# Optimization experiments

Hardware: AMD Instinct MI355X
Metric: run time of the kernel (lower is better)

## Reference

```python
import jax, jax.numpy as jnp
import numpy as np

D_MODEL = 1024
N_HEADS = 16
SEQ_LEN = 2048
BATCH = 2
NEG = -1.0e9


def sinusoidal_embeddings(seq_len, d_k):
    # Faithful to the torch version: row 0 is all zeros; even cols get sin,
    # odd cols get cos of position/theta (theta uses the SAME index j, not j//2).
    theta = 10000.0 ** (2.0 * jnp.arange(d_k, dtype=jnp.float32) / d_k)  # [d_k]
    pos = jnp.arange(1, seq_len, dtype=jnp.float32)[:, None] / theta      # [S-1, d_k]
    even = (jnp.arange(d_k) % 2 == 0)
    body = jnp.where(even, jnp.sin(pos), jnp.cos(pos))                    # [S-1, d_k]
    return jnp.concatenate([jnp.zeros((1, d_k), dtype=pos.dtype), body], axis=0)


def setup_inputs() -> dict:
    key = jax.random.key(0)
    k_x, k_q, k_k, k_v, k_o = jax.random.split(key, 5)
    scale = 0.02
    return {
        "X": jax.random.normal(k_x, (BATCH, SEQ_LEN, D_MODEL), dtype=jnp.float32),
        "W_q": jax.random.normal(k_q, (D_MODEL, D_MODEL), dtype=jnp.float32) * scale,
        "W_k": jax.random.normal(k_k, (D_MODEL, D_MODEL), dtype=jnp.float32) * scale,
        "W_v": jax.random.normal(k_v, (D_MODEL, D_MODEL), dtype=jnp.float32) * scale,
        "W_o": jax.random.normal(k_o, (D_MODEL, D_MODEL), dtype=jnp.float32) * scale,
    }


def reference(X, W_q, W_k, W_v, W_o):
    B, S, D = X.shape
    H, d_k = N_HEADS, D // N_HEADS

    def proj(W):  # nn.Linear (no bias): y = x @ W.T, then split heads -> [B,H,S,d_k]
        return (X @ W.T).reshape(B, S, H, d_k).transpose(0, 2, 1, 3)

    Q, K, V = proj(W_q), proj(W_k), proj(W_v)

    pos = sinusoidal_embeddings(S, d_k)          # [S, d_k]
    Q = Q + pos
    K = K + pos

    mask = jnp.triu(jnp.full((S, S), NEG, dtype=X.dtype), k=1)  # [S,S]
    scores = jnp.einsum("bhqd,bhkd->bhqk", Q, K) / jnp.sqrt(jnp.float32(d_k)) + mask
    weights = jax.nn.softmax(scores, axis=-1)
    attn = jnp.einsum("bhqk,bhkd->bhqd", weights, V)            # [B,H,S,d_k]

    attn = attn.transpose(0, 2, 1, 3).reshape(B, S, D)
    return attn @ W_o.T + X
```

## Files before the change

### kernel.cpp

```cpp
#include <hip/hip_runtime.h>
#include <hip/hip_bf16.h>
#include <math.h>

#define S_LEN 2048
#define DMODEL 1024
#define NHEADS 16
#define DHEAD 64
#define NBATCH 2
#define MROWS (NBATCH * S_LEN)

typedef float f32x4 __attribute__((ext_vector_type(4)));
typedef unsigned short u16x8 __attribute__((ext_vector_type(8)));
typedef __bf16 bf16x8 __attribute__((ext_vector_type(8)));

__device__ __forceinline__ f32x4 mfma16(u16x8 a, u16x8 b, f32x4 c) {
    return __builtin_amdgcn_mfma_f32_16x16x32_bf16(
        __builtin_bit_cast(bf16x8, a), __builtin_bit_cast(bf16x8, b), c, 0, 0, 0);
}

__device__ __forceinline__ unsigned short f2bf(float f) {
    unsigned int u = __builtin_bit_cast(unsigned int, f);
    u += 0x7FFFu + ((u >> 16) & 1u);
    return (unsigned short)(u >> 16);
}

__device__ __forceinline__ unsigned int cvtpk(float lo, float hi) {
    unsigned int r;
    asm("v_cvt_pk_bf16_f32 %0, %1, %2" : "=v"(r) : "v"(lo), "v"(hi));
    return r;
}

__device__ __forceinline__ void gl16(const void* g, void* l) {
    __builtin_amdgcn_global_load_lds(
        (const __attribute__((address_space(1))) unsigned int*)g,
        (__attribute__((address_space(3))) unsigned int*)l, 16, 0, 0);
}

#define PIPE_BAR_12() do { \
    asm volatile("s_waitcnt vmcnt(12)" ::: "memory"); \
    __builtin_amdgcn_sched_barrier(0); \
    __builtin_amdgcn_s_barrier(); \
    __builtin_amdgcn_sched_barrier(0); } while (0)
#define PIPE_BAR_0() do { \
    asm volatile("s_waitcnt vmcnt(0)" ::: "memory"); \
    __builtin_amdgcn_sched_barrier(0); \
    __builtin_amdgcn_s_barrier(); \
    __builtin_amdgcn_sched_barrier(0); } while (0)

__global__ __launch_bounds__(256) void cvt5(
    const float* __restrict__ X, const float* __restrict__ Wq,
    const float* __restrict__ Wk, const float* __restrict__ Wv,
    const float* __restrict__ Wo,
    unsigned short* __restrict__ Xbf, unsigned short* __restrict__ Wbf,
    float* __restrict__ pos)
{
    int b = blockIdx.x;
    if (b >= 4096) {
        int i = (b - 4096) * 256 + threadIdx.x;
        int s = i >> 6, d = i & 63;
        float theta = powf(10000.0f, (2.0f * (float)d) / 64.0f);
        float x = (float)s / theta;
        float v = (d & 1) ? cosf(x) : sinf(x);
        pos[i] = (s == 0) ? 0.0f : v;
        return;
    }
    const float* s; unsigned short* d; int t;
    if (b < 2048) { s = X; d = Xbf; t = b * 256 + threadIdx.x; }
    else {
        int z = (b - 2048) >> 9, bb = (b - 2048) & 511;
        s = (z == 0) ? Wq : (z == 1) ? Wk : (z == 2) ? Wv : Wo;
        d = Wbf + (z << 20);
        t = bb * 256 + threadIdx.x;
    }
    float4 a = *((const float4*)s + t * 2);
    float4 c = *((const float4*)s + t * 2 + 1);
    u16x8 o;
    o[0] = f2bf(a.x); o[1] = f2bf(a.y); o[2] = f2bf(a.z); o[3] = f2bf(a.w);
    o[4] = f2bf(c.x); o[5] = f2bf(c.y); o[6] = f2bf(c.z); o[7] = f2bf(c.w);
    *((u16x8*)d + t) = o;
}

__global__ __launch_bounds__(512) void gemm_qkv(
    const unsigned short* __restrict__ Xbf, const unsigned short* __restrict__ Wbf,
    const float* __restrict__ pos,
    unsigned short* __restrict__ qb, unsigned short* __restrict__ kb,
    unsigned short* __restrict__ vt)
{
    const int y = blockIdx.y;
    const int z = y >> 2;
    const unsigned short* __restrict__ W = Wbf + (z << 20);
    __shared__ unsigned short L[2][32768];
    const int t = threadIdx.x;
    const int lane = t & 63;
    const int w = t >> 6;
    const int wm = w >> 2, wn = w & 3;
    const int m0 = blockIdx.x * 256;
    const int nb = (y & 3) * 256;
    const int ll = lane & 15, lg = lane >> 4;
    const int tr = t >> 3;
    const int ch = (t & 7) ^ (tr & 7);

    f32x4 acc[8][4] = {};

    const unsigned short* gA[4];
    const unsigned short* gB[4];
    #pragma unroll
    for (int i = 0; i < 4; i++) {
        gA[i] = Xbf + (m0 + i * 64 + tr) * 1024 + ch * 8;
        gB[i] = W + (nb + i * 64 + tr) * 1024 + ch * 8;
    }

    const int sw0 = ((0 * 4 + lg) ^ (ll & 7)) * 16;
    const int sw1 = ((1 * 4 + lg) ^ (ll & 7)) * 16;
    const int aBase = (wm * 128 + ll) * 128;
    const int bBase = 32768 + (wn * 64 + ll) * 128;

    auto sqA01 = [&](unsigned short* Ln) {
        gl16(gA[0], Ln + (0 * 64 + w * 8) * 64); gA[0] += 64;
        gl16(gA[1], Ln + (1 * 64 + w * 8) * 64); gA[1] += 64;
    };
    auto sqA23 = [&](unsigned short* Ln) {
        gl16(gA[2], Ln + (2 * 64 + w * 8) * 64); gA[2] += 64;
        gl16(gA[3], Ln + (3 * 64 + w * 8) * 64); gA[3] += 64;
    };
    auto sqB01 = [&](unsigned short* Ln) {
        gl16(gB[0], Ln + 16384 + (0 * 64 + w * 8) * 64); gB[0] += 64;
        gl16(gB[1], Ln + 16384 + (1 * 64 + w * 8) * 64); gB[1] += 64;
    };
    auto sqB23 = [&](unsigned short* Ln) {
        gl16(gB[2], Ln + 16384 + (2 * 64 + w * 8) * 64); gB[2] += 64;
        gl16(gB[3], Ln + 16384 + (3 * 64 + w * 8) * 64); gB[3] += 64;
    };

    u16x8 bf[4][2];

    auto quad = [&](int q, const char* bA) {
        const char* pa = bA + aBase + q * 4096;
        u16x8 a00 = *(const u16x8*)(pa + sw0);
        u16x8 a01 = *(const u16x8*)(pa + sw1);
        u16x8 a10 = *(const u16x8*)(pa + 2048 + sw0);
        u16x8 a11 = *(const u16x8*)(pa + 2048 + sw1);
        __builtin_amdgcn_s_setprio(1);
        #pragma unroll
        for (int nf = 0; nf < 4; nf++) {
            acc[q * 2 + 0][nf] = mfma16(a00, bf[nf][0], acc[q * 2 + 0][nf]);
            acc[q * 2 + 1][nf] = mfma16(a10, bf[nf][0], acc[q * 2 + 1][nf]);
        }
        #pragma unroll
        for (int nf = 0; nf < 4; nf++) {
            acc[q * 2 + 0][nf] = mfma16(a01, bf[nf][1], acc[q * 2 + 0][nf]);
            acc[q * 2 + 1][nf] = mfma16(a11, bf[nf][1], acc[q * 2 + 1][nf]);
        }
        __builtin_amdgcn_s_setprio(0);
    };

    auto ktile = [&](const unsigned short* Lb, unsigned short* Ln, bool stg) {
        const char* bA = (const char*)Lb;
        const char* bB = (const char*)Lb;
        if (stg) sqA01(Ln);
        #pragma unroll
        for (int nf = 0; nf < 4; nf++) {
            const char* p = bB + bBase + nf * 2048;
            bf[nf][0] = *(const u16x8*)(p + sw0);
            bf[nf][1] = *(const u16x8*)(p + sw1);
        }
        quad(0, bA);
        __builtin_amdgcn_s_barrier();
        if (stg) sqA23(Ln);
        quad(1, bA);
        __builtin_amdgcn_s_barrier();
        if (stg) sqB01(Ln);
        quad(2, bA);
        __builtin_amdgcn_s_barrier();
        if (stg) sqB23(Ln);
        quad(3, bA);
        PIPE_BAR_0();
    };

    sqA01(L[0]); sqA23(L[0]); sqB01(L[0]); sqB23(L[0]);
    PIPE_BAR_0();
    #pragma unroll 1
    for (int tt = 0; tt < 8; tt++) {
        ktile(L[0], L[1], true);
        ktile(L[1], L[0], tt != 7);
    }

    if (z == 2) {
        #pragma unroll
        for (int mf = 0; mf < 8; mf++) {
            const int row0 = m0 + wm * 128 + mf * 16 + lg * 4;
            const int b = row0 >> 11, s0 = row0 & 2047;
            #pragma unroll
            for (int nf = 0; nf < 4; nf++) {
                const int c = nb + wn * 64 + nf * 16 + ll;
                const int h = c >> 6, d = c & 63;
                unsigned long long pk =
                    (unsigned long long)cvtpk(acc[mf][nf][0], acc[mf][nf][1]) |
                    ((unsigned long long)cvtpk(acc[mf][nf][2], acc[mf][nf][3]) << 32);
                *(unsigned long long*)&vt[(((b * NHEADS + h) * 64) + d) * S_LEN + s0] = pk;
            }
        }
    } else {
        unsigned short* const dst = (z == 0) ? qb : kb;
        #pragma unroll
        for (int mf = 0; mf < 8; mf++) {
            #pragma unroll
            for (int nf = 0; nf < 4; nf++) {
                #pragma unroll
                for (int r = 0; r < 4; r++) {
                    const int row = m0 + wm * 128 + mf * 16 + lg * 4 + r;
                    const int c = nb + wn * 64 + nf * 16 + ll;
                    const int b = row >> 11, s = row & 2047;
                    const int h = c >> 6, d = c & 63;
                    float v = acc[mf][nf][r] + pos[s * 64 + d];
                    if (z == 0) v *= 0.1803368801111244f;
                    dst[(((b * NHEADS + h) * S_LEN) + s) * 64 + d] = f2bf(v);
                }
            }
        }
    }
}

__global__ __launch_bounds__(512, 4) void attn_kernel(
    const unsigned short* __restrict__ qb,
    const unsigned short* __restrict__ kb,
    const unsigned short* __restrict__ vt,
    unsigned short* __restrict__ attnb)
{
    __shared__ unsigned short Klds[2][128 * 64];
    __shared__ unsigned short Vlds[2][64 * 128];
    __shared__ unsigned short Plds[8][16 * 64];

    const int bh = blockIdx.y;
    const int x = blockIdx.x;
    const int qt = (bh < 16) ? (15 - x) : x;

    const int lane = threadIdx.x & 63;
    const int w = threadIdx.x >> 6;
    const int lg = lane >> 4, ll = lane & 15;
    const int r8 = lane >> 3, ch = (lane & 7) ^ r8;
    const int r4 = lane >> 4, c16 = lane & 15;

    const unsigned short* Q = qb + bh * (S_LEN * 64);
    const unsigned short* K = kb + bh * (S_LEN * 64);
    const unsigned short* V = vt + bh * (64 * S_LEN);
    const int q0 = qt * 128 + w * 16;

    u16x8 qf0 = *(const u16x8*)(Q + (q0 + ll) * 64 + lg * 8);
    u16x8 qf1 = *(const u16x8*)(Q + (q0 + ll) * 64 + 32 + lg * 8);

    f32x4 o_acc[4] = {};
    float l_part = 0.0f;

    const int sw0 = ((0 * 4 + lg) ^ (ll & 7)) * 16;
    const int sw1 = ((1 * 4 + lg) ^ (ll & 7)) * 16;
    const char* kb0p0 = (const char*)&Klds[0][0] + ll * 128 + sw0;
    const char* kb0p1 = (const char*)&Klds[0][0] + ll * 128 + sw1;
    const char* kb1p0 = (const char*)&Klds[1][0] + ll * 128 + sw0;
    const char* kb1p1 = (const char*)&Klds[1][0] + ll * 128 + sw1;
    const char* vb0p0 = (const char*)&Vlds[0][0] + ll * 256 + sw0;
    const char* vb0p1 = (const char*)&Vlds[0][0] + ll * 256 + sw1;
    const char* vb1p0 = (const char*)&Vlds[1][0] + ll * 256 + sw0;
    const char* vb1p1 = (const char*)&Vlds[1][0] + ll * 256 + sw1;
    const int E = (ll & 7) << 4;
    char* pwb = (char*)&Plds[w][0] + (((ll * 128) + lg * 8) ^ (E & 16));
    const int pw_o0 = 0 ^ (E & 96), pw_o1 = 32 ^ (E & 96);
    const int pw_o2 = 64 ^ (E & 96), pw_o3 = 96 ^ (E & 96);
    const char* pr0 = (const char*)&Plds[w][0] + ll * 128 + sw0;
    const char* pr1 = (const char*)&Plds[w][0] + ll * 128 + sw1;
    unsigned short* kd0 = &Klds[0][(w * 16) * 64];
    unsigned short* kd1 = &Klds[1][(w * 16) * 64];
    unsigned short* vd0 = &Vlds[0][(w * 8) * 128];
    unsigned short* vd1 = &Vlds[1][(w * 8) * 128];
    const unsigned short* gk  = K + (w * 16 + r8) * 64 + ch * 8;
    const unsigned short* gva = V + (w * 8 + r4) * S_LEN + ((c16 ^ r4) * 8);
    const unsigned short* gvb = V + (w * 8 + 4 + r4) * S_LEN + ((c16 ^ (4 + r4)) * 8);
    const int dthr = w * 16 + ll - lg * 4;

    auto stage2 = [&](unsigned short* kd, unsigned short* vd) {
        gl16(gk, kd);
        gl16(gk + 512, kd + 512);
        gl16(gva, vd);
        gl16(gvb, vd + 512);
        gk += 128 * 64;
        gva += 128;
        gvb += 128;
    };

    auto tile_body = [&](const char* kp0, const char* kp1,
                         const char* vp0, const char* vp1, bool masked, int thr) {
        f32x4 sc[4] = {};
        __builtin_amdgcn_s_setprio(1);
        #pragma unroll
        for (int f = 0; f < 4; f++) {
            const u16x8 kfa = *(const u16x8*)(kp0 + f * 2048);
            sc[f] = mfma16(kfa, qf0, sc[f]);
            const u16x8 kfb = *(const u16x8*)(kp1 + f * 2048);
            sc[f] = mfma16(kfb, qf1, sc[f]);
        }
        __builtin_amdgcn_s_setprio(0);
        if (masked) {
            #pragma unroll
            for (int f = 0; f < 4; f++)
                #pragma unroll
                for (int r = 0; r < 4; r++)
                    if (f * 16 + r > thr) sc[f][r] = -1.0e9f;
        }
        float ts = 0.0f;
        #pragma unroll
        for (int f = 0; f < 4; f++)
            #pragma unroll
            for (int r = 0; r < 4; r++) {
                const float p = __builtin_amdgcn_exp2f(sc[f][r]);
                sc[f][r] = p;
                ts += p;
            }
        l_part += ts;
        *(unsigned long long*)(pwb + pw_o0) =
            (unsigned long long)cvtpk(sc[0][0], sc[0][1]) | ((unsigned long long)cvtpk(sc[0][2], sc[0][3]) << 32);
        *(unsigned long long*)(pwb + pw_o1) =
            (unsigned long long)cvtpk(sc[1][0], sc[1][1]) | ((unsigned long long)cvtpk(sc[1][2], sc[1][3]) << 32);
        *(unsigned long long*)(pwb + pw_o2) =
            (unsigned long long)cvtpk(sc[2][0], sc[2][1]) | ((unsigned long long)cvtpk(sc[2][2], sc[2][3]) << 32);
        *(unsigned long long*)(pwb + pw_o3) =
            (unsigned long long)cvtpk(sc[3][0], sc[3][1]) | ((unsigned long long)cvtpk(sc[3][2], sc[3][3]) << 32);
        const u16x8 pf0 = *(const u16x8*)pr0;
        const u16x8 pf1 = *(const u16x8*)pr1;
        __builtin_amdgcn_s_setprio(1);
        #pragma unroll
        for (int f = 0; f < 4; f++) {
            o_acc[f] = mfma16(pf0, *(const u16x8*)(vp0 + f * 4096), o_acc[f]);
            o_acc[f] = mfma16(pf1, *(const u16x8*)(vp1 + f * 4096), o_acc[f]);
        }
        __builtin_amdgcn_s_setprio(0);
    };

    auto body128_full = [&](const char* kp0, const char* kp1,
                            const char* vp0, const char* vp1) {
        tile_body(kp0, kp1, vp0, vp1, false, 0);
        tile_body(kp0 + 8192, kp1 + 8192, vp0 + 128, vp1 + 128, false, 0);
    };
    auto body128_diag = [&](const char* kp0, const char* kp1,
                            const char* vp0, const char* vp1) {
        tile_body(kp0, kp1, vp0, vp1, true, dthr);
        if (w >= 4)
            tile_body(kp0 + 8192, kp1 + 8192, vp0 + 128, vp1 + 128, true, dthr - 64);
    };

    stage2(kd0, vd0);
    __syncthreads();

    int p = 0;
    while (p + 2 <= qt) {
        stage2(kd1, vd1);
        body128_full(kb0p0, kb0p1, vb0p0, vb0p1);
        __syncthreads();
        stage2(kd0, vd0);
        body128_full(kb1p0, kb1p1, vb1p0, vb1p1);
        __syncthreads();
        p += 2;
    }
    if (p < qt) {
        stage2(kd1, vd1);
        body128_full(kb0p0, kb0p1, vb0p0, vb0p1);
        __syncthreads();
        body128_diag(kb1p0, kb1p1, vb1p0, vb1p1);
    } else {
        body128_diag(kb0p0, kb0p1, vb0p0, vb0p1);
    }

    l_part += __shfl_xor(l_part, 16);
    l_part += __shfl_xor(l_part, 32);

    const int bb = bh >> 4, h = bh & 15;
    float lr0 = 1.0f / __shfl(l_part, lg * 4 + 0);
    float lr1 = 1.0f / __shfl(l_part, lg * 4 + 1);
    float lr2 = 1.0f / __shfl(l_part, lg * 4 + 2);
    float lr3 = 1.0f / __shfl(l_part, lg * 4 + 3);
    #pragma unroll
    for (int f = 0; f < 4; f++) {
        const int colbase = h * 64 + f * 16 + ll;
        attnb[(bb * S_LEN + q0 + lg * 4 + 0) * DMODEL + colbase] = f2bf(o_acc[f][0] * lr0);
        attnb[(bb * S_LEN + q0 + lg * 4 + 1) * DMODEL + colbase] = f2bf(o_acc[f][1] * lr1);
        attnb[(bb * S_LEN + q0 + lg * 4 + 2) * DMODEL + colbase] = f2bf(o_acc[f][2] * lr2);
        attnb[(bb * S_LEN + q0 + lg * 4 + 3) * DMODEL + colbase] = f2bf(o_acc[f][3] * lr3);
    }
}

__global__ __launch_bounds__(128) void gemm_out(
    const unsigned short* __restrict__ Abf,
    const unsigned short* __restrict__ Wbf,
    const float* __restrict__ X,
    float* __restrict__ out)
{
    const unsigned short* __restrict__ W = Wbf + (3u << 20);
    __shared__ unsigned short L[3][192 * 64];
    const int t = threadIdx.x;
    const int lane = t & 63;
    const int w = t >> 6;
    const int m0 = blockIdx.x * 128;
    const int n0 = blockIdx.y * 64;
    const int ll = lane & 15, lg = lane >> 4;
    const int r8 = lane >> 3, ch = (lane & 7) ^ r8;

    f32x4 acc[4][4] = {};

    const unsigned short* gA[8];
    const unsigned short* gB[4];
    #pragma unroll
    for (int i = 0; i < 8; i++) gA[i] = Abf + (m0 + w * 64 + i * 8 + r8) * 1024 + ch * 8;
    #pragma unroll
    for (int i = 0; i < 4; i++) gB[i] = W + (n0 + w * 32 + i * 8 + r8) * 1024 + ch * 8;

    const int sw0 = ((0 * 4 + lg) ^ (ll & 7)) * 16;
    const int sw1 = ((1 * 4 + lg) ^ (ll & 7)) * 16;

    auto stage = [&](unsigned short* Lb) {
        unsigned short* const dA = Lb + (w * 64) * 64;
        unsigned short* const dB = Lb + 128 * 64 + (w * 32) * 64;
        #pragma unroll
        for (int i = 0; i < 8; i++) { gl16(gA[i], dA + i * 8 * 64); gA[i] += 64; }
        #pragma unroll
        for (int i = 0; i < 4; i++) { gl16(gB[i], dB + i * 8 * 64); gB[i] += 64; }
    };
    auto compute = [&](const unsigned short* Lb) {
        const char* const pA0 = (const char*)Lb + (w * 64 + ll) * 128 + sw0;
        const char* const pA1 = (const char*)Lb + (w * 64 + ll) * 128 + sw1;
        const char* const pB0 = (const char*)Lb + 16384 + ll * 128 + sw0;
        const char* const pB1 = (const char*)Lb + 16384 + ll * 128 + sw1;
        u16x8 af[4], bfv[4];
        #pragma unroll
        for (int m = 0; m < 4; m++) af[m] = *(const u16x8*)(pA0 + m * 2048);
        #pragma unroll
        for (int n = 0; n < 4; n++) bfv[n] = *(const u16x8*)(pB0 + n * 2048);
        __builtin_amdgcn_s_setprio(1);
        #pragma unroll
        for (int m = 0; m < 4; m++)
            #pragma unroll
            for (int n = 0; n < 4; n++)
                acc[m][n] = mfma16(af[m], bfv[n], acc[m][n]);
        __builtin_amdgcn_s_setprio(0);
        #pragma unroll
        for (int m = 0; m < 4; m++) af[m] = *(const u16x8*)(pA1 + m * 2048);
        #pragma unroll
        for (int n = 0; n < 4; n++) bfv[n] = *(const u16x8*)(pB1 + n * 2048);
        __builtin_amdgcn_s_setprio(1);
        #pragma unroll
        for (int m = 0; m < 4; m++)
            #pragma unroll
            for (int n = 0; n < 4; n++)
                acc[m][n] = mfma16(af[m], bfv[n], acc[m][n]);
        __builtin_amdgcn_s_setprio(0);
    };

    stage(L[0]);
    stage(L[1]);
    PIPE_BAR_12();
    for (int tt = 0; tt < 4; tt++) {
        stage(L[2]); compute(L[0]); PIPE_BAR_12();
        stage(L[0]); compute(L[1]); PIPE_BAR_12();
        stage(L[1]); compute(L[2]); PIPE_BAR_12();
    }
    stage(L[2]); compute(L[0]); PIPE_BAR_12();
    stage(L[0]); compute(L[1]); PIPE_BAR_12();
    compute(L[2]); PIPE_BAR_0();
    compute(L[0]);

    #pragma unroll
    for (int m = 0; m < 4; m++)
        #pragma unroll
        for (int n = 0; n < 4; n++)
            #pragma unroll
            for (int r = 0; r < 4; r++) {
                const int row = m0 + w * 64 + m * 16 + lg * 4 + r;
                const int col = n0 + n * 16 + ll;
                out[row * 1024 + col] = acc[m][n][r] + X[row * 1024 + col];
            }
}

extern "C" void kernel_launch(void* const* d_in, const int* in_sizes, int n_in,
                              void* d_out, int out_size, void* d_ws, size_t ws_size,
                              hipStream_t stream) {
    const float* X  = (const float*)d_in[0];
    const float* Wq = (const float*)d_in[1];
    const float* Wk = (const float*)d_in[2];
    const float* Wv = (const float*)d_in[3];
    const float* Wo = (const float*)d_in[4];
    float* out = (float*)d_out;

    char* ws = (char*)d_ws;
    float*          pos  = (float*)(ws);
    unsigned short* Xbf  = (unsigned short*)(ws + (512u << 10));
    unsigned short* Wbf  = (unsigned short*)(ws + (512u << 10) + (8u  << 20));
    unsigned short* qb   = (unsigned short*)(ws + (512u << 10) + (16u << 20));
    unsigned short* kb   = (unsigned short*)(ws + (512u << 10) + (24u << 20));
    unsigned short* vt   = (unsigned short*)(ws + (512u << 10) + (32u << 20));
    unsigned short* attb = Xbf;

    cvt5<<<dim3(4608), dim3(256), 0, stream>>>(X, Wq, Wk, Wv, Wo, Xbf, Wbf, pos);
    gemm_qkv<<<dim3(16, 12), dim3(512), 0, stream>>>(Xbf, Wbf, pos, qb, kb, vt);
    attn_kernel<<<dim3(16, 32), dim3(512), 0, stream>>>(qb, kb, vt, attb);
    gemm_out<<<dim3(32, 16), dim3(128), 0, stream>>>(attb, Wbf, X, out);
}
```

Baseline: 95.79 us.

## Reorder GEMM LDS staging to wait on partial vmcnt instead of full drain

Restructures the double-buffered K-loop of the projection GEMM so global-to-LDS loads are issued B first, then A row blocks in the order the compute quads consume them. This lets each barrier wait with a partial vmcnt (2 or 6) instead of draining all loads, so the last A block can still be in flight into the next tile. The loop is flattened to 15 iterations plus a peeled epilogue tile. Correctness now depends on the exact vmcnt accounting matching the issue order of the loads.

New measurement: 95.42 us. No clear change (-0.4%).

```diff
diff --git a/kernel.cpp b/kernel.cpp
--- a/kernel.cpp
+++ b/kernel.cpp
@@ -36,6 +36,11 @@
         (__attribute__((address_space(3))) unsigned int*)l, 16, 0, 0);
 }
 
+#define VMB(N) do { \
+    asm volatile("s_waitcnt vmcnt(" #N ")" ::: "memory"); \
+    __builtin_amdgcn_sched_barrier(0); \
+    __builtin_amdgcn_s_barrier(); \
+    __builtin_amdgcn_sched_barrier(0); } while (0)
 #define PIPE_BAR_12() do { \
     asm volatile("s_waitcnt vmcnt(12)" ::: "memory"); \
     __builtin_amdgcn_sched_barrier(0); \
@@ -114,26 +119,34 @@
     const int sw1 = ((1 * 4 + lg) ^ (ll & 7)) * 16;
     const int aBase = (wm * 128 + ll) * 128;
     const int bBase = 32768 + (wn * 64 + ll) * 128;
-
-    auto sqA01 = [&](unsigned short* Ln) {
-        gl16(gA[0], Ln + (0 * 64 + w * 8) * 64); gA[0] += 64;
-        gl16(gA[1], Ln + (1 * 64 + w * 8) * 64); gA[1] += 64;
-    };
-    auto sqA23 = [&](unsigned short* Ln) {
-        gl16(gA[2], Ln + (2 * 64 + w * 8) * 64); gA[2] += 64;
-        gl16(gA[3], Ln + (3 * 64 + w * 8) * 64); gA[3] += 64;
-    };
-    auto sqB01 = [&](unsigned short* Ln) {
-        gl16(gB[0], Ln + 16384 + (0 * 64 + w * 8) * 64); gB[0] += 64;
-        gl16(gB[1], Ln + 16384 + (1 * 64 + w * 8) * 64); gB[1] += 64;
-    };
-    auto sqB23 = [&](unsigned short* Ln) {
-        gl16(gB[2], Ln + 16384 + (2 * 64 + w * 8) * 64); gB[2] += 64;
-        gl16(gB[3], Ln + 16384 + (3 * 64 + w * 8) * 64); gB[3] += 64;
+    const int wdst = w * 8 * 64;
+
+    auto stB01 = [&](unsigned short* Ln) {
+        gl16(gB[0], Ln + 16384 + wdst);          gB[0] += 64;
+        gl16(gB[1], Ln + 16384 + 4096 + wdst);   gB[1] += 64;
+    };
+    auto stB23 = [&](unsigned short* Ln) {
+        gl16(gB[2], Ln + 16384 + 8192 + wdst);   gB[2] += 64;
+        gl16(gB[3], Ln + 16384 + 12288 + wdst);  gB[3] += 64;
+    };
+    auto stA02 = [&](unsigned short* Ln) {
+        gl16(gA[0], Ln + wdst);                  gA[0] += 64;
+        gl16(gA[2], Ln + 8192 + wdst);           gA[2] += 64;
+    };
+    auto stA13 = [&](unsigned short* Ln) {
+        gl16(gA[1], Ln + 4096 + wdst);           gA[1] += 64;
+        gl16(gA[3], Ln + 12288 + wdst);          gA[3] += 64;
     };
 
     u16x8 bf[4][2];
-
+    auto loadB = [&](const char* bB) {
+        #pragma unroll
+        for (int nf = 0; nf < 4; nf++) {
+            const char* p = bB + bBase + nf * 2048;
+            bf[nf][0] = *(const u16x8*)(p + sw0);
+            bf[nf][1] = *(const u16x8*)(p + sw1);
+        }
+    };
     auto quad = [&](int q, const char* bA) {
         const char* pa = bA + aBase + q * 4096;
         u16x8 a00 = *(const u16x8*)(pa + sw0);
@@ -154,35 +167,37 @@
         __builtin_amdgcn_s_setprio(0);
     };
 
-    auto ktile = [&](const unsigned short* Lb, unsigned short* Ln, bool stg) {
-        const char* bA = (const char*)Lb;
-        const char* bB = (const char*)Lb;
-        if (stg) sqA01(Ln);
-        #pragma unroll
-        for (int nf = 0; nf < 4; nf++) {
-            const char* p = bB + bBase + nf * 2048;
-            bf[nf][0] = *(const u16x8*)(p + sw0);
-            bf[nf][1] = *(const u16x8*)(p + sw1);
-        }
+    stB01(L[0]); stB23(L[0]); stA02(L[0]); stA13(L[0]);
+    VMB(2);
+
+    #pragma unroll 1
+    for (int tt = 0; tt < 15; tt++) {
+        const char* bA = (const char*)L[tt & 1];
+        unsigned short* Ln = L[(tt + 1) & 1];
+        stB01(Ln);
+        loadB(bA);
         quad(0, bA);
         __builtin_amdgcn_s_barrier();
-        if (stg) sqA23(Ln);
+        stB23(Ln);
         quad(1, bA);
         __builtin_amdgcn_s_barrier();
-        if (stg) sqB01(Ln);
+        stA02(Ln);
+        VMB(6);
         quad(2, bA);
         __builtin_amdgcn_s_barrier();
-        if (stg) sqB23(Ln);
+        stA13(Ln);
         quad(3, bA);
-        PIPE_BAR_0();
-    };
-
-    sqA01(L[0]); sqA23(L[0]); sqB01(L[0]); sqB23(L[0]);
-    PIPE_BAR_0();
-    #pragma unroll 1
-    for (int tt = 0; tt < 8; tt++) {
-        ktile(L[0], L[1], true);
-        ktile(L[1], L[0], tt != 7);
+        VMB(2);
+    }
+    {
+        const char* bA = (const char*)L[1];
+        loadB(bA);
+        quad(0, bA);
+        __builtin_amdgcn_s_barrier();
+        quad(1, bA);
+        VMB(0);
+        quad(2, bA);
+        quad(3, bA);
     }
 
     if (z == 2) {
```
